# Kernel optimization log

Measured on AMD Instinct MI355X. Metric: run time of the kernel, lower is better.

The kernel has to match this reference:

```python
import jax, jax.numpy as jnp
import numpy as np

TOKENS = 16384
HIDDEN = 2048
FFN = 8192


def setup_inputs() -> dict:
    key = jax.random.key(0)
    k_x, k_w1, k_w2 = jax.random.split(key, 3)
    x = jax.random.normal(k_x, (TOKENS, HIDDEN), dtype=jnp.float32)
    # PyTorch Linear default init scale ~ 1/sqrt(fan_in); use small scale for stability
    w1 = jax.random.normal(k_w1, (HIDDEN, FFN), dtype=jnp.float32) * (1.0 / np.sqrt(HIDDEN))
    b1 = jnp.zeros((FFN,), dtype=jnp.float32)
    w2 = jax.random.normal(k_w2, (FFN, HIDDEN), dtype=jnp.float32) * (1.0 / np.sqrt(FFN))
    b2 = jnp.zeros((HIDDEN,), dtype=jnp.float32)
    return {"x": x, "w1": w1, "b1": b1, "w2": w2, "b2": b2}


def reference(x, w1, b1, w2, b2):
    # all_to_all with equal split sizes on a single group is an identity
    # permutation of token chunks; on one device it is exactly identity.
    # dispatch (identity) -> MLP -> combine (identity)
    h = jax.nn.gelu(x @ w1 + b1, approximate=False)  # (tokens, ffn), exact erf GELU as torch nn.GELU
    y = h @ w2 + b2  # (tokens, hidden)
    return y
```

## Files before the change

### kernel.cpp

```cpp
#include <hip/hip_runtime.h>
#include <hip/hip_bf16.h>
#include <cstdint>
#include <cstddef>

typedef __bf16 bf16_t;
typedef __bf16 bf16x8 __attribute__((ext_vector_type(8)));
typedef float  f32x4  __attribute__((ext_vector_type(4)));

#define TOKENS 16384
#define HIDDEN 2048
#define FFN    8192

__device__ __forceinline__ void gload_lds16(const bf16_t* g, bf16_t* l) {
    __builtin_amdgcn_global_load_lds((const __attribute__((address_space(1))) void*)g,
                                     (__attribute__((address_space(3))) void*)l,
                                     16, 0, 0);
}

__global__ void cvt_f32_to_bf16(const float* __restrict__ in, bf16_t* __restrict__ out, int n8) {
    int i = blockIdx.x * blockDim.x + threadIdx.x;
    if (i >= n8) return;
    size_t base = (size_t)i * 8;
    f32x4 v0 = *(const f32x4*)&in[base];
    f32x4 v1 = *(const f32x4*)&in[base + 4];
    bf16x8 o;
    o[0] = (bf16_t)v0[0]; o[1] = (bf16_t)v0[1]; o[2] = (bf16_t)v0[2]; o[3] = (bf16_t)v0[3];
    o[4] = (bf16_t)v1[0]; o[5] = (bf16_t)v1[1]; o[6] = (bf16_t)v1[2]; o[7] = (bf16_t)v1[3];
    *(bf16x8*)&out[base] = o;
}

__global__ void transpose_cvt(const float* __restrict__ src, bf16_t* __restrict__ dst,
                              int R, int C) {
    __shared__ bf16_t tile[64][66];
    const int tcols = C >> 6;
    const int bx = blockIdx.x % tcols;
    const int by = blockIdx.x / tcols;
    const int c0 = bx << 6, r0 = by << 6;
    const int t = threadIdx.x;
#pragma unroll
    for (int i = 0; i < 16; ++i) {
        int idx = i * 256 + t;
        int rr = idx >> 6, cc = idx & 63;
        tile[rr][cc] = (bf16_t)src[(size_t)(r0 + rr) * C + (c0 + cc)];
    }
    __syncthreads();
#pragma unroll
    for (int i = 0; i < 16; ++i) {
        int idx = i * 256 + t;
        int cc = idx >> 6, rr = idx & 63;
        dst[(size_t)(c0 + cc) * R + (r0 + rr)] = tile[rr][cc];
    }
}

#define BAR() __builtin_amdgcn_s_barrier()
#define LGKM0() do { asm volatile("s_waitcnt lgkmcnt(0)" ::: "memory"); \
                     __builtin_amdgcn_sched_barrier(0); } while (0)
#define VMW(n) asm volatile("s_waitcnt vmcnt(" #n ")" ::: "memory")
#define PRIO1() __builtin_amdgcn_s_setprio(1)
#define PRIO0() __builtin_amdgcn_s_setprio(0)

#define DS_A(BUF, QM) do { \
    _Pragma("unroll") for (int mf = 0; mf < 4; ++mf) \
    _Pragma("unroll") for (int ks = 0; ks < 2; ++ks) \
        af[mf][ks] = *(const bf16x8*)&smem[(BUF)*16384 + wr*8192 + (((QM)*4+mf)*2+ks)*512 + lnb_e]; \
} while (0)

#define DS_B(BUF, QN, BB) do { \
    _Pragma("unroll") for (int nf = 0; nf < 2; ++nf) \
    _Pragma("unroll") for (int ks = 0; ks < 2; ++ks) \
        BB[nf][ks] = *(const bf16x8*)&smem[32768 + (BUF)*16384 + bhalf + (((QN)*2+nf)*2+ks)*512 + lnb_e]; \
} while (0)

#define MFMA_Q(QM, QN, BB) do { \
    _Pragma("unroll") for (int ks = 0; ks < 2; ++ks) \
    _Pragma("unroll") for (int mf = 0; mf < 4; ++mf) \
    _Pragma("unroll") for (int nf = 0; nf < 2; ++nf) \
        acc[(QM)*4+mf][(QN)*2+nf] = __builtin_amdgcn_mfma_f32_16x16x32_bf16( \
            af[mf][ks], BB[nf][ks], acc[(QM)*4+mf][(QN)*2+nf], 0, 0, 0); \
} while (0)

#define STAGE(GBASE, HROWS, TILE, EOFF) do { \
    gload_lds16((GBASE) + aoff0 + (size_t)(HROWS) * K + (TILE) * 64, \
                &smem[(EOFF) + wave * 512]); \
    gload_lds16((GBASE) + aoff1 + (size_t)(HROWS) * K + (TILE) * 64, \
                &smem[(EOFF) + 4096 + wave * 512]); \
} while (0)

template<bool GELU_EPI, int M, int N, int K>
__global__ __launch_bounds__(512, 2)
void gemm8p(const bf16_t* __restrict__ A, const bf16_t* __restrict__ BT,
            const float* __restrict__ bias, void* __restrict__ out)
{
    constexpr int BM = 256, BN = 256;
    constexpr int NT = K / 64, NI = NT / 2;
    constexpr int NBN = N / BN;
    __shared__ __align__(128) bf16_t smem[65536];

    const int t = threadIdx.x;
    const int wave = t >> 6, lane = t & 63;
    const int fr = lane & 15, fq = lane >> 4;
    const int wr = wave >> 2, wc = wave & 3;

    int wg = blockIdx.x;
    { const int cpx = (int)gridDim.x >> 3; wg = (wg & 7) * cpx + (wg >> 3); }
    const int bm = wg / NBN, bn = wg % NBN;
    const int rowA0 = bm * BM, colB0 = bn * BN;

    int sr0, sk0, sr1, sk1;
    {
        int o = t * 16;
        int ri = (o >> 6) & 15;
        int b = (o & 63) ^ ((ri & 8) << 2);
        sr0 = ((o >> 10) >> 1) * 16 + ri;
        sk0 = ((o >> 10) & 1) * 32 + (b >> 1);
        o = 8192 + t * 16;
        ri = (o >> 6) & 15;
        b = (o & 63) ^ ((ri & 8) << 2);
        sr1 = ((o >> 10) >> 1) * 16 + ri;
        sk1 = ((o >> 10) & 1) * 32 + (b >> 1);
    }
    const bf16_t* gA0 = A + (size_t)rowA0 * K;
    const bf16_t* gB0 = BT + (size_t)colB0 * K;
    const size_t aoff0 = (size_t)sr0 * K + sk0;
    const size_t aoff1 = (size_t)sr1 * K + sk1;

    const int lnb_e = fr * 32 + ((fq * 8) ^ ((fr & 8) << 1));
    const int bhalf = (wc >> 1) * 8192 + (wc & 1) * 4096;

    f32x4 acc[8][4] = {};
    bf16x8 af[4][2], b0[2][2], b1[2][2];

    STAGE(gA0, 0,   0, 0);
    STAGE(gA0, 128, 0, 8192);
    STAGE(gB0, 0,   0, 32768);
    STAGE(gB0, 128, 0, 40960);
    STAGE(gA0, 0,   1, 16384);
    STAGE(gB0, 0,   1, 49152);
    STAGE(gB0, 128, 1, 57344);
    VMW(6);
    BAR();

    for (int i = 0; i < NI - 1; ++i) {
        const int t1 = 2 * i + 1, t2 = 2 * i + 2, t3 = 2 * i + 3;
        DS_A(0, 0); DS_B(0, 0, b0);
        STAGE(gA0, 128, t1, 24576);
        BAR(); LGKM0();
        PRIO1(); MFMA_Q(0, 0, b0); PRIO0();
        BAR();
        DS_B(0, 1, b1);
        BAR(); LGKM0();
        PRIO1(); MFMA_Q(0, 1, b1); PRIO0();
        BAR();
        DS_A(0, 1);
        STAGE(gB0, 0, t2, 32768);
        BAR(); LGKM0();
        PRIO1(); MFMA_Q(1, 1, b1); PRIO0();
        BAR();
        STAGE(gB0, 128, t2, 40960);
        STAGE(gA0, 0,   t2, 0);
        VMW(6);
        BAR();
        PRIO1(); MFMA_Q(1, 0, b0); PRIO0();
        BAR();
        DS_A(1, 0); DS_B(1, 0, b0);
        STAGE(gA0, 128, t2, 8192);
        BAR(); LGKM0();
        PRIO1(); MFMA_Q(0, 0, b0); PRIO0();
        BAR();
        DS_B(1, 1, b1);
        BAR(); LGKM0();
        PRIO1(); MFMA_Q(0, 1, b1); PRIO0();
        BAR();
        DS_A(1, 1);
        STAGE(gB0, 0, t3, 49152);
        BAR(); LGKM0();
        PRIO1(); MFMA_Q(1, 1, b1); PRIO0();
        BAR();
        STAGE(gB0, 128, t3, 57344);
        STAGE(gA0, 0,   t3, 16384);
        VMW(6);
        BAR();
        PRIO1(); MFMA_Q(1, 0, b0); PRIO0();
        BAR();
    }

    DS_A(0, 0); DS_B(0, 0, b0);
    STAGE(gA0, 128, NT - 1, 24576);
    BAR(); LGKM0();
    PRIO1(); MFMA_Q(0, 0, b0); PRIO0();
    BAR();
    DS_B(0, 1, b1);
    BAR(); LGKM0();
    PRIO1(); MFMA_Q(0, 1, b1); PRIO0();
    BAR();
    DS_A(0, 1);
    BAR(); LGKM0();
    PRIO1(); MFMA_Q(1, 1, b1); PRIO0();
    BAR();
    VMW(0);
    BAR();
    PRIO1(); MFMA_Q(1, 0, b0); PRIO0();
    BAR();
    DS_A(1, 0); DS_B(1, 0, b0);
    BAR(); LGKM0();
    PRIO1(); MFMA_Q(0, 0, b0); PRIO0();
    BAR();
    DS_B(1, 1, b1);
    BAR(); LGKM0();
    PRIO1(); MFMA_Q(0, 1, b1); PRIO0();
    BAR();
    DS_A(1, 1);
    BAR(); LGKM0();
    PRIO1(); MFMA_Q(1, 1, b1); PRIO0();
    MFMA_Q(1, 0, b0);

    const int orow = rowA0 + wr * 128 + fq * 4;
    const int ocol = colB0 + wc * 64 + fr;
#pragma unroll
    for (int mf = 0; mf < 8; ++mf) {
#pragma unroll
        for (int nf = 0; nf < 4; ++nf) {
            const int c = ocol + nf * 16;
            const float bv = bias[c];
#pragma unroll
            for (int v = 0; v < 4; ++v) {
                const int r = orow + mf * 16 + v;
                float xv = acc[mf][nf][v] + bv;
                if constexpr (GELU_EPI) {
                    float g = 0.5f * xv * (1.0f + erff(xv * 0.70710678118654752f));
                    ((bf16_t*)out)[(size_t)r * N + c] = (bf16_t)g;
                } else {
                    ((float*)out)[(size_t)r * N + c] = xv;
                }
            }
        }
    }
}

extern "C" void kernel_launch(void* const* d_in, const int* in_sizes, int n_in,
                              void* d_out, int out_size, void* d_ws, size_t ws_size,
                              hipStream_t stream) {
    const float* x  = (const float*)d_in[0];
    const float* w1 = (const float*)d_in[1];
    const float* b1 = (const float*)d_in[2];
    const float* w2 = (const float*)d_in[3];
    const float* b2 = (const float*)d_in[4];
    float* y = (float*)d_out;

    const size_t xb_elems  = (size_t)TOKENS * HIDDEN;
    const size_t w1t_elems = (size_t)FFN * HIDDEN;
    const size_t w2t_elems = (size_t)HIDDEN * FFN;
    const size_t h_elems   = (size_t)TOKENS * FFN;
    const size_t need = (xb_elems + w1t_elems + w2t_elems + h_elems) * sizeof(bf16_t);
    if (ws_size < need) return;

    char* ws = (char*)d_ws;
    bf16_t* xb  = (bf16_t*)ws;
    bf16_t* w1t = xb + xb_elems;
    bf16_t* w2t = w1t + w1t_elems;
    bf16_t* h   = w2t + w2t_elems;

    cvt_f32_to_bf16<<<(TOKENS * HIDDEN / 8 + 255) / 256, 256, 0, stream>>>(
        x, xb, TOKENS * HIDDEN / 8);
    transpose_cvt<<<(HIDDEN / 64) * (FFN / 64), 256, 0, stream>>>(w1, w1t, HIDDEN, FFN);
    transpose_cvt<<<(FFN / 64) * (HIDDEN / 64), 256, 0, stream>>>(w2, w2t, FFN, HIDDEN);

    gemm8p<true, TOKENS, FFN, HIDDEN>
        <<<(TOKENS / 256) * (FFN / 256), 512, 0, stream>>>(xb, w1t, b1, h);
    gemm8p<false, TOKENS, HIDDEN, FFN>
        <<<(TOKENS / 256) * (HIDDEN / 256), 512, 0, stream>>>(h, w2t, b2, y);
}
```

Baseline: 1.102 ms.

## Replace 8-phase ping-pong GEMM schedule with 2-barrier per-tile double buffering

Restructures the main K-loop of both GEMMs. The old schedule interleaved quarter-tile LDS reads, partial global stages and MFMA quadrants across eight barrier-separated phases. The new one waits for a whole K-tile, reads all A and B fragments at once, runs three MFMA quadrants, then issues the full next-tile prefetch before the last quadrant. This cuts barriers and explicit lgkmcnt waits per tile. In exchange it needs a second A-fragment register set, which adds register pressure under 2-waves-per-SIMD launch bounds. It also overlaps global loads with less compute.

```diff
diff --git a/kernel.cpp b/kernel.cpp
--- a/kernel.cpp
+++ b/kernel.cpp
@@ -53,30 +53,35 @@
 }
 
 #define BAR() __builtin_amdgcn_s_barrier()
-#define LGKM0() do { asm volatile("s_waitcnt lgkmcnt(0)" ::: "memory"); \
-                     __builtin_amdgcn_sched_barrier(0); } while (0)
+#define SB0() __builtin_amdgcn_sched_barrier(0)
 #define VMW(n) asm volatile("s_waitcnt vmcnt(" #n ")" ::: "memory")
 #define PRIO1() __builtin_amdgcn_s_setprio(1)
 #define PRIO0() __builtin_amdgcn_s_setprio(0)
 
-#define DS_A(BUF, QM) do { \
+#define DS_A0(BUF) do { \
     _Pragma("unroll") for (int mf = 0; mf < 4; ++mf) \
     _Pragma("unroll") for (int ks = 0; ks < 2; ++ks) \
-        af[mf][ks] = *(const bf16x8*)&smem[(BUF)*16384 + wr*8192 + (((QM)*4+mf)*2+ks)*512 + lnb_e]; \
-} while (0)
-
-#define DS_B(BUF, QN, BB) do { \
+        afA[mf][ks] = *(const bf16x8*)&smem[(BUF)*16384 + wr*8192 + ((mf)*2+ks)*512 + lnb_e]; \
+} while (0)
+
+#define DS_A1(BUF) do { \
+    _Pragma("unroll") for (int mf = 0; mf < 4; ++mf) \
+    _Pragma("unroll") for (int ks = 0; ks < 2; ++ks) \
+        afB[mf][ks] = *(const bf16x8*)&smem[(BUF)*16384 + wr*8192 + ((4+mf)*2+ks)*512 + lnb_e]; \
+} while (0)
+
+#define DS_Bm(BUF, QN, BB) do { \
     _Pragma("unroll") for (int nf = 0; nf < 2; ++nf) \
     _Pragma("unroll") for (int ks = 0; ks < 2; ++ks) \
         BB[nf][ks] = *(const bf16x8*)&smem[32768 + (BUF)*16384 + bhalf + (((QN)*2+nf)*2+ks)*512 + lnb_e]; \
 } while (0)
 
-#define MFMA_Q(QM, QN, BB) do { \
+#define MFMA_Q(QM, QN, AF, BB) do { \
     _Pragma("unroll") for (int ks = 0; ks < 2; ++ks) \
     _Pragma("unroll") for (int mf = 0; mf < 4; ++mf) \
     _Pragma("unroll") for (int nf = 0; nf < 2; ++nf) \
         acc[(QM)*4+mf][(QN)*2+nf] = __builtin_amdgcn_mfma_f32_16x16x32_bf16( \
-            af[mf][ks], BB[nf][ks], acc[(QM)*4+mf][(QN)*2+nf], 0, 0, 0); \
+            AF[mf][ks], BB[nf][ks], acc[(QM)*4+mf][(QN)*2+nf], 0, 0, 0); \
 } while (0)
 
 #define STAGE(GBASE, HROWS, TILE, EOFF) do { \
@@ -86,9 +91,29 @@
                 &smem[(EOFF) + 4096 + wave * 512]); \
 } while (0)
 
+#define STAGE_TILE(TILE, ABASE, BBASE) do { \
+    STAGE(gA0, 0,   TILE, (ABASE));         \
+    STAGE(gA0, 128, TILE, (ABASE) + 8192);  \
+    STAGE(gB0, 0,   TILE, (BBASE));         \
+    STAGE(gB0, 128, TILE, (BBASE) + 8192);  \
+} while (0)
+
+#define TILE_C(BUF, VN, STAGE_STMT) do { \
+    VMW(VN); BAR(); SB0(); \
+    DS_A0(BUF); DS_Bm(BUF, 0, b0); DS_Bm(BUF, 1, b1); DS_A1(BUF); \
+    PRIO1(); \
+    MFMA_Q(0, 0, afA, b0); \
+    MFMA_Q(0, 1, afA, b1); \
+    MFMA_Q(1, 1, afB, b1); \
+    PRIO0(); \
+    BAR(); SB0(); \
+    STAGE_STMT; \
+    PRIO1(); MFMA_Q(1, 0, afB, b0); PRIO0(); \
+} while (0)
+
 template<bool GELU_EPI, int M, int N, int K>
 __global__ __launch_bounds__(512, 2)
-void gemm8p(const bf16_t* __restrict__ A, const bf16_t* __restrict__ BT,
+void gemm2b(const bf16_t* __restrict__ A, const bf16_t* __restrict__ BT,
             const float* __restrict__ bias, void* __restrict__ out)
 {
     constexpr int BM = 256, BN = 256;
@@ -128,91 +153,18 @@
     const int bhalf = (wc >> 1) * 8192 + (wc & 1) * 4096;
 
     f32x4 acc[8][4] = {};
-    bf16x8 af[4][2], b0[2][2], b1[2][2];
-
-    STAGE(gA0, 0,   0, 0);
-    STAGE(gA0, 128, 0, 8192);
-    STAGE(gB0, 0,   0, 32768);
-    STAGE(gB0, 128, 0, 40960);
-    STAGE(gA0, 0,   1, 16384);
-    STAGE(gB0, 0,   1, 49152);
-    STAGE(gB0, 128, 1, 57344);
-    VMW(6);
-    BAR();
+    bf16x8 afA[4][2], afB[4][2], b0[2][2], b1[2][2];
+
+    STAGE_TILE(0, 0, 32768);
+    STAGE_TILE(1, 16384, 49152);
 
     for (int i = 0; i < NI - 1; ++i) {
-        const int t1 = 2 * i + 1, t2 = 2 * i + 2, t3 = 2 * i + 3;
-        DS_A(0, 0); DS_B(0, 0, b0);
-        STAGE(gA0, 128, t1, 24576);
-        BAR(); LGKM0();
-        PRIO1(); MFMA_Q(0, 0, b0); PRIO0();
-        BAR();
-        DS_B(0, 1, b1);
-        BAR(); LGKM0();
-        PRIO1(); MFMA_Q(0, 1, b1); PRIO0();
-        BAR();
-        DS_A(0, 1);
-        STAGE(gB0, 0, t2, 32768);
-        BAR(); LGKM0();
-        PRIO1(); MFMA_Q(1, 1, b1); PRIO0();
-        BAR();
-        STAGE(gB0, 128, t2, 40960);
-        STAGE(gA0, 0,   t2, 0);
-        VMW(6);
-        BAR();
-        PRIO1(); MFMA_Q(1, 0, b0); PRIO0();
-        BAR();
-        DS_A(1, 0); DS_B(1, 0, b0);
-        STAGE(gA0, 128, t2, 8192);
-        BAR(); LGKM0();
-        PRIO1(); MFMA_Q(0, 0, b0); PRIO0();
-        BAR();
-        DS_B(1, 1, b1);
-        BAR(); LGKM0();
-        PRIO1(); MFMA_Q(0, 1, b1); PRIO0();
-        BAR();
-        DS_A(1, 1);
-        STAGE(gB0, 0, t3, 49152);
-        BAR(); LGKM0();
-        PRIO1(); MFMA_Q(1, 1, b1); PRIO0();
-        BAR();
-        STAGE(gB0, 128, t3, 57344);
-        STAGE(gA0, 0,   t3, 16384);
-        VMW(6);
-        BAR();
-        PRIO1(); MFMA_Q(1, 0, b0); PRIO0();
-        BAR();
-    }
-
-    DS_A(0, 0); DS_B(0, 0, b0);
-    STAGE(gA0, 128, NT - 1, 24576);
-    BAR(); LGKM0();
-    PRIO1(); MFMA_Q(0, 0, b0); PRIO0();
-    BAR();
-    DS_B(0, 1, b1);
-    BAR(); LGKM0();
-    PRIO1(); MFMA_Q(0, 1, b1); PRIO0();
-    BAR();
-    DS_A(0, 1);
-    BAR(); LGKM0();
-    PRIO1(); MFMA_Q(1, 1, b1); PRIO0();
-    BAR();
-    VMW(0);
-    BAR();
-    PRIO1(); MFMA_Q(1, 0, b0); PRIO0();
-    BAR();
-    DS_A(1, 0); DS_B(1, 0, b0);
-    BAR(); LGKM0();
-    PRIO1(); MFMA_Q(0, 0, b0); PRIO0();
-    BAR();
-    DS_B(1, 1, b1);
-    BAR(); LGKM0();
-    PRIO1(); MFMA_Q(0, 1, b1); PRIO0();
-    BAR();
-    DS_A(1, 1);
-    BAR(); LGKM0();
-    PRIO1(); MFMA_Q(1, 1, b1); PRIO0();
-    MFMA_Q(1, 0, b0);
+        const int s0 = 2 * i + 2, s1 = 2 * i + 3;
+        TILE_C(0, 8, STAGE_TILE(s0, 0, 32768));
+        TILE_C(1, 8, STAGE_TILE(s1, 16384, 49152));
+    }
+    TILE_C(0, 8, ((void)0));
+    TILE_C(1, 0, ((void)0));
 
     const int orow = rowA0 + wr * 128 + fq * 4;
     const int ocol = colB0 + wc * 64 + fr;
@@ -265,8 +217,8 @@
     transpose_cvt<<<(HIDDEN / 64) * (FFN / 64), 256, 0, stream>>>(w1, w1t, HIDDEN, FFN);
     transpose_cvt<<<(FFN / 64) * (HIDDEN / 64), 256, 0, stream>>>(w2, w2t, FFN, HIDDEN);
 
-    gemm8p<true, TOKENS, FFN, HIDDEN>
+    gemm2b<true, TOKENS, FFN, HIDDEN>
         <<<(TOKENS / 256) * (FFN / 256), 512, 0, stream>>>(xb, w1t, b1, h);
-    gemm8p<false, TOKENS, HIDDEN, FFN>
+    gemm2b<false, TOKENS, HIDDEN, FFN>
         <<<(TOKENS / 256) * (HIDDEN / 256), 512, 0, stream>>>(h, w2t, b2, y);
 }
```

New measurement: 1.348 ms. 22.3% more time.

## Software-pipeline LDS fragment reads with double-buffered registers and partial lgkmcnt waits

Applied to the files above, without the earlier changes.

Adds a second set of A and B fragment registers so the LDS reads for the next MFMA quadrant are issued before the current quadrant's MFMAs run. The full lgkmcnt(0) waits are replaced by partial waits that only cover the fragments the next MFMA block needs. The intent is to hide LDS read latency behind matrix work inside the 8-phase GEMM loop. The cost is higher VGPR pressure from the extra fragment buffers, which could cause spills or lower occupancy at 512 threads with 2 blocks per CU. The waitcnt counts must exactly match the order in which loads are issued.

```diff
diff --git a/kernel.cpp b/kernel.cpp
--- a/kernel.cpp
+++ b/kernel.cpp
@@ -53,30 +53,30 @@
 }
 
 #define BAR() __builtin_amdgcn_s_barrier()
-#define LGKM0() do { asm volatile("s_waitcnt lgkmcnt(0)" ::: "memory"); \
-                     __builtin_amdgcn_sched_barrier(0); } while (0)
+#define SB0() __builtin_amdgcn_sched_barrier(0)
+#define LGKMW(n) do { asm volatile("s_waitcnt lgkmcnt(" #n ")" ::: "memory"); SB0(); } while (0)
 #define VMW(n) asm volatile("s_waitcnt vmcnt(" #n ")" ::: "memory")
 #define PRIO1() __builtin_amdgcn_s_setprio(1)
 #define PRIO0() __builtin_amdgcn_s_setprio(0)
 
-#define DS_A(BUF, QM) do { \
+#define DS_A(BUF, QM, AF) do { \
     _Pragma("unroll") for (int mf = 0; mf < 4; ++mf) \
     _Pragma("unroll") for (int ks = 0; ks < 2; ++ks) \
-        af[mf][ks] = *(const bf16x8*)&smem[(BUF)*16384 + wr*8192 + (((QM)*4+mf)*2+ks)*512 + lnb_e]; \
-} while (0)
-
-#define DS_B(BUF, QN, BB) do { \
+        AF[mf][ks] = *(const bf16x8*)&smem[(BUF)*16384 + wr*8192 + (((QM)*4+mf)*2+ks)*512 + lnb_e]; \
+} while (0)
+
+#define DS_Bm(BUF, QN, BB) do { \
     _Pragma("unroll") for (int nf = 0; nf < 2; ++nf) \
     _Pragma("unroll") for (int ks = 0; ks < 2; ++ks) \
         BB[nf][ks] = *(const bf16x8*)&smem[32768 + (BUF)*16384 + bhalf + (((QN)*2+nf)*2+ks)*512 + lnb_e]; \
 } while (0)
 
-#define MFMA_Q(QM, QN, BB) do { \
+#define MFMA_Q(QM, QN, AF, BB) do { \
     _Pragma("unroll") for (int ks = 0; ks < 2; ++ks) \
     _Pragma("unroll") for (int mf = 0; mf < 4; ++mf) \
     _Pragma("unroll") for (int nf = 0; nf < 2; ++nf) \
         acc[(QM)*4+mf][(QN)*2+nf] = __builtin_amdgcn_mfma_f32_16x16x32_bf16( \
-            af[mf][ks], BB[nf][ks], acc[(QM)*4+mf][(QN)*2+nf], 0, 0, 0); \
+            AF[mf][ks], BB[nf][ks], acc[(QM)*4+mf][(QN)*2+nf], 0, 0, 0); \
 } while (0)
 
 #define STAGE(GBASE, HROWS, TILE, EOFF) do { \
@@ -88,7 +88,7 @@
 
 template<bool GELU_EPI, int M, int N, int K>
 __global__ __launch_bounds__(512, 2)
-void gemm8p(const bf16_t* __restrict__ A, const bf16_t* __restrict__ BT,
+void gemmpl(const bf16_t* __restrict__ A, const bf16_t* __restrict__ BT,
             const float* __restrict__ bias, void* __restrict__ out)
 {
     constexpr int BM = 256, BN = 256;
@@ -128,7 +128,7 @@
     const int bhalf = (wc >> 1) * 8192 + (wc & 1) * 4096;
 
     f32x4 acc[8][4] = {};
-    bf16x8 af[4][2], b0[2][2], b1[2][2];
+    bf16x8 afA[4][2], afB[4][2], bA[2][2], bB[2][2];
 
     STAGE(gA0, 0,   0, 0);
     STAGE(gA0, 128, 0, 8192);
@@ -139,80 +139,85 @@
     STAGE(gB0, 128, 1, 57344);
     VMW(6);
     BAR();
+    DS_A(0, 0, afA); DS_Bm(0, 0, bA);
 
     for (int i = 0; i < NI - 1; ++i) {
         const int t1 = 2 * i + 1, t2 = 2 * i + 2, t3 = 2 * i + 3;
-        DS_A(0, 0); DS_B(0, 0, b0);
+        DS_Bm(0, 1, bB);
         STAGE(gA0, 128, t1, 24576);
-        BAR(); LGKM0();
-        PRIO1(); MFMA_Q(0, 0, b0); PRIO0();
-        BAR();
-        DS_B(0, 1, b1);
-        BAR(); LGKM0();
-        PRIO1(); MFMA_Q(0, 1, b1); PRIO0();
-        BAR();
-        DS_A(0, 1);
+        BAR(); LGKMW(4);
+        PRIO1(); MFMA_Q(0, 0, afA, bA); PRIO0();
+        BAR();
+        DS_A(0, 1, afB);
+        BAR(); LGKMW(8);
+        PRIO1(); MFMA_Q(0, 1, afA, bB); PRIO0();
+        BAR();
         STAGE(gB0, 0, t2, 32768);
-        BAR(); LGKM0();
-        PRIO1(); MFMA_Q(1, 1, b1); PRIO0();
+        BAR(); LGKMW(0);
+        PRIO1(); MFMA_Q(1, 1, afB, bB); PRIO0();
         BAR();
         STAGE(gB0, 128, t2, 40960);
         STAGE(gA0, 0,   t2, 0);
         VMW(6);
         BAR();
-        PRIO1(); MFMA_Q(1, 0, b0); PRIO0();
-        BAR();
-        DS_A(1, 0); DS_B(1, 0, b0);
+        DS_A(1, 0, afA); DS_Bm(1, 0, bB);
+        LGKMW(12);
+        PRIO1(); MFMA_Q(1, 0, afB, bA); PRIO0();
+        BAR();
+        DS_Bm(1, 1, bA);
         STAGE(gA0, 128, t2, 8192);
-        BAR(); LGKM0();
-        PRIO1(); MFMA_Q(0, 0, b0); PRIO0();
-        BAR();
-        DS_B(1, 1, b1);
-        BAR(); LGKM0();
-        PRIO1(); MFMA_Q(0, 1, b1); PRIO0();
-        BAR();
-        DS_A(1, 1);
+        BAR(); LGKMW(4);
+        PRIO1(); MFMA_Q(0, 0, afA, bB); PRIO0();
+        BAR();
+        DS_A(1, 1, afB);
+        BAR(); LGKMW(8);
+        PRIO1(); MFMA_Q(0, 1, afA, bA); PRIO0();
+        BAR();
         STAGE(gB0, 0, t3, 49152);
-        BAR(); LGKM0();
-        PRIO1(); MFMA_Q(1, 1, b1); PRIO0();
+        BAR(); LGKMW(0);
+        PRIO1(); MFMA_Q(1, 1, afB, bA); PRIO0();
         BAR();
         STAGE(gB0, 128, t3, 57344);
         STAGE(gA0, 0,   t3, 16384);
         VMW(6);
         BAR();
-        PRIO1(); MFMA_Q(1, 0, b0); PRIO0();
-        BAR();
-    }
-
-    DS_A(0, 0); DS_B(0, 0, b0);
+        DS_A(0, 0, afA); DS_Bm(0, 0, bA);
+        LGKMW(12);
+        PRIO1(); MFMA_Q(1, 0, afB, bB); PRIO0();
+        BAR();
+    }
+
+    DS_Bm(0, 1, bB);
     STAGE(gA0, 128, NT - 1, 24576);
-    BAR(); LGKM0();
-    PRIO1(); MFMA_Q(0, 0, b0); PRIO0();
-    BAR();
-    DS_B(0, 1, b1);
-    BAR(); LGKM0();
-    PRIO1(); MFMA_Q(0, 1, b1); PRIO0();
-    BAR();
-    DS_A(0, 1);
-    BAR(); LGKM0();
-    PRIO1(); MFMA_Q(1, 1, b1); PRIO0();
+    BAR(); LGKMW(4);
+    PRIO1(); MFMA_Q(0, 0, afA, bA); PRIO0();
+    BAR();
+    DS_A(0, 1, afB);
+    BAR(); LGKMW(8);
+    PRIO1(); MFMA_Q(0, 1, afA, bB); PRIO0();
+    BAR();
+    BAR(); LGKMW(0);
+    PRIO1(); MFMA_Q(1, 1, afB, bB); PRIO0();
     BAR();
     VMW(0);
     BAR();
-    PRIO1(); MFMA_Q(1, 0, b0); PRIO0();
-    BAR();
-    DS_A(1, 0); DS_B(1, 0, b0);
-    BAR(); LGKM0();
-    PRIO1(); MFMA_Q(0, 0, b0); PRIO0();
-    BAR();
-    DS_B(1, 1, b1);
-    BAR(); LGKM0();
-    PRIO1(); MFMA_Q(0, 1, b1); PRIO0();
-    BAR();
-    DS_A(1, 1);
-    BAR(); LGKM0();
-    PRIO1(); MFMA_Q(1, 1, b1); PRIO0();
-    MFMA_Q(1, 0, b0);
+    DS_A(1, 0, afA); DS_Bm(1, 0, bB);
+    LGKMW(12);
+    PRIO1(); MFMA_Q(1, 0, afB, bA); PRIO0();
+    BAR();
+    DS_Bm(1, 1, bA);
+    BAR(); LGKMW(4);
+    PRIO1(); MFMA_Q(0, 0, afA, bB); PRIO0();
+    BAR();
+    DS_A(1, 1, afB);
+    BAR(); LGKMW(8);
+    PRIO1(); MFMA_Q(0, 1, afA, bA); PRIO0();
+    BAR();
+    BAR(); LGKMW(0);
+    PRIO1(); MFMA_Q(1, 1, afB, bA); PRIO0();
+    BAR();
+    LGKMW(0);
+    PRIO1(); MFMA_Q(1, 0, afB, bB); PRIO0();
 
     const int orow = rowA0 + wr * 128 + fq * 4;
     const int ocol = colB0 + wc * 64 + fr;
@@ -265,8 +270,8 @@
     transpose_cvt<<<(HIDDEN / 64) * (FFN / 64), 256, 0, stream>>>(w1, w1t, HIDDEN, FFN);
     transpose_cvt<<<(FFN / 64) * (HIDDEN / 64), 256, 0, stream>>>(w2, w2t, FFN, HIDDEN);
 
-    gemm8p<true, TOKENS, FFN, HIDDEN>
+    gemmpl<true, TOKENS, FFN, HIDDEN>
         <<<(TOKENS / 256) * (FFN / 256), 512, 0, stream>>>(xb, w1t, b1, h);
-    gemm8p<false, TOKENS, HIDDEN, FFN>
+    gemmpl<false, TOKENS, HIDDEN, FFN>
         <<<(TOKENS / 256) * (HIDDEN / 256), 512, 0, stream>>>(h, w2t, b2, y);
 }
```

Measured after the change: 2.009 ms. 82.3% more time.
